# Optimization experiments

Hardware: AMD Instinct MI355X
Metric: run time of the kernel (lower is better)

## Reference

```python
import jax, jax.numpy as jnp
import numpy as np

T, H, E, F, K, FS = 2048, 2048, 64, 512, 8, 512


def setup_inputs() -> dict:
    key = jax.random.key(0)
    ks = jax.random.split(key, 6)
    s = 0.02
    return {
        "hidden_states": jax.random.normal(ks[0], (T, H), jnp.float32),
        # merged gate: E router logits + 1 shared-expert gate logit
        "W_gate": jax.random.normal(ks[1], (H, E + 1), jnp.float32) * s,
        # per-expert merged gate_up proj: [E, H, 2F]
        "W_gate_up": jax.random.normal(ks[2], (E, H, 2 * F), jnp.float32) * s,
        "W_down": jax.random.normal(ks[3], (E, F, H), jnp.float32) * s,
        # shared expert
        "Ws_gate_up": jax.random.normal(ks[4], (H, 2 * FS), jnp.float32) * s,
        "Ws_down": jax.random.normal(ks[5], (FS, H), jnp.float32) * s,
    }


def reference(hidden_states, W_gate, W_gate_up, W_down, Ws_gate_up, Ws_down):
    x = hidden_states  # [T, H]
    logits_all = x @ W_gate                      # [T, E+1]
    router_logits = logits_all[:, :E]
    shared_gate_logit = logits_all[:, E:]        # [T, 1]

    # FusedMoE routing: softmax -> top_k -> renormalize (norm_topk_prob=True)
    probs = jax.nn.softmax(router_logits.astype(jnp.float32), axis=-1)
    topk_w, topk_idx = jax.lax.top_k(probs, K)   # [T, K]
    topk_w = topk_w / jnp.sum(topk_w, axis=-1, keepdims=True)
    # dense combine weights [T, E] (zero for unselected experts)
    combine = jnp.zeros((T, E), probs.dtype).at[
        jnp.arange(T)[:, None], topk_idx].set(topk_w)

    # grouped expert GEMMs (dense reference: every expert sees all tokens,
    # combine-weights zero-out unrouted pairs)
    gu = jnp.einsum('th,ehf->etf', x, W_gate_up)   # [E, T, 2F]
    g, u = jnp.split(gu, 2, axis=-1)
    act = jax.nn.silu(g) * u                       # [E, T, F]
    # apply combine weight before down-proj to avoid [E, T, H] intermediate
    act = act * combine.T[:, :, None].astype(act.dtype)
    routed = jnp.einsum('etf,efh->th', act, W_down)  # [T, H]

    # shared expert (Qwen3NextMLP with sigmoid expert_gate)
    sgu = x @ Ws_gate_up                           # [T, 2FS]
    sg, su = jnp.split(sgu, 2, axis=-1)
    shared = (jax.nn.silu(sg) * su) @ Ws_down      # [T, H]
    shared = jax.nn.sigmoid(shared_gate_logit) * shared

    return shared + routed.astype(x.dtype)
```

## Files before the change

### kernel.cpp

```cpp
#include <hip/hip_runtime.h>
#include <hip/hip_bf16.h>
#include <math.h>

#define T_TOK 2048
#define H_DIM 2048
#define E_NUM 64
#define F_DIM 512
#define K_TOP 8
#define FS_DIM 512
#define NROWS (T_TOK * K_TOP)

typedef __attribute__((ext_vector_type(8))) short short8v;
typedef __attribute__((ext_vector_type(4))) float f32x4;

static __device__ __forceinline__ unsigned short f2bf(float f) {
    unsigned int u = __float_as_uint(f);
    u += 0x7fff + ((u >> 16) & 1);
    return (unsigned short)(u >> 16);
}

#define BCHUNK(row, k8) ((((k8) ^ ((row) + ((row) >> 3)))) & 7)
#define ASWZ(row) (((row) + ((row) >> 3)) & 7)

typedef const unsigned int __attribute__((address_space(1))) gu32;
typedef unsigned int __attribute__((address_space(3))) lu32;
#define GLDS16(gsrc, ldst) \
    __builtin_amdgcn_global_load_lds((gu32*)(gsrc), (lu32*)(ldst), 16, 0, 0)

__global__ __launch_bounds__(256) void cvt_bf16_kernel(
    const float* __restrict__ in, unsigned short* __restrict__ out, int n8)
{
    int i = blockIdx.x * 256 + threadIdx.x;
    if (i < n8) {
        const float4* p = (const float4*)(in + (size_t)i * 8);
        float4 v0 = p[0], v1 = p[1];
        ushort4 a = make_ushort4(f2bf(v0.x), f2bf(v0.y), f2bf(v0.z), f2bf(v0.w));
        ushort4 b = make_ushort4(f2bf(v1.x), f2bf(v1.y), f2bf(v1.z), f2bf(v1.w));
        ushort4* q = (ushort4*)(out + (size_t)i * 8);
        q[0] = a; q[1] = b;
    }
}

__global__ __launch_bounds__(64) void router_kernel(
    const float* __restrict__ x, const float* __restrict__ Wg,
    int* __restrict__ topk_idx, float* __restrict__ topk_w,
    float* __restrict__ sgate, int* __restrict__ counts)
{
    const int t = blockIdx.x;
    const int lane = threadIdx.x;
    const float* xr = x + (size_t)t * H_DIM;

    float a0 = 0.f, a1 = 0.f, a2 = 0.f, a3 = 0.f;
    for (int h = 0; h < H_DIM; h += 4) {
        float4 xv = *(const float4*)&xr[h];
        a0 += xv.x * Wg[(h + 0) * 65 + lane];
        a1 += xv.y * Wg[(h + 1) * 65 + lane];
        a2 += xv.z * Wg[(h + 2) * 65 + lane];
        a3 += xv.w * Wg[(h + 3) * 65 + lane];
    }
    float logit = (a0 + a1) + (a2 + a3);

    float a64 = 0.f;
    for (int h = lane; h < H_DIM; h += 64) a64 += xr[h] * Wg[h * 65 + 64];
#pragma unroll
    for (int off = 32; off >= 1; off >>= 1) a64 += __shfl_xor(a64, off);

    float v = logit;
    float selv[K_TOP]; int seli[K_TOP];
#pragma unroll
    for (int k = 0; k < K_TOP; ++k) {
        float mv = v; int mi = lane;
#pragma unroll
        for (int off = 32; off >= 1; off >>= 1) {
            float ov = __shfl_xor(mv, off);
            int   oi = __shfl_xor(mi, off);
            if (ov > mv || (ov == mv && oi < mi)) { mv = ov; mi = oi; }
        }
        selv[k] = mv; seli[k] = mi;
        if (lane == mi) v = -INFINITY;
    }

    if (lane == 0) {
        float m = selv[0];
        float w[K_TOP]; float s = 0.f;
#pragma unroll
        for (int k = 0; k < K_TOP; ++k) { w[k] = __expf(selv[k] - m); s += w[k]; }
        float inv = 1.f / s;
#pragma unroll
        for (int k = 0; k < K_TOP; ++k) {
            topk_idx[t * K_TOP + k] = seli[k];
            topk_w[t * K_TOP + k] = w[k] * inv;
            atomicAdd(&counts[seli[k]], 1);
        }
        sgate[t] = 1.f / (1.f + __expf(-a64));
    }
}

__global__ __launch_bounds__(256) void bucket_kernel(
    const int* __restrict__ topk_idx, const float* __restrict__ topk_w,
    const int* __restrict__ counts, int* __restrict__ offsets,
    int* __restrict__ bucket_tok, float* __restrict__ bucket_w)
{
    const int e = blockIdx.x, thr = threadIdx.x;
    __shared__ int cnt[256];
    __shared__ int base_s;
    const int q0 = thr * 64;
    int c = 0;
    for (int q = 0; q < 64; ++q) c += (topk_idx[q0 + q] == e) ? 1 : 0;
    cnt[thr] = c;
    __syncthreads();
    if (thr == 0) {
        int off = 0;
        for (int i = 0; i < e; ++i) off += counts[i];
        offsets[e] = off;
        base_s = off;
        int run = 0;
        for (int i = 0; i < 256; ++i) { int tval = cnt[i]; cnt[i] = run; run += tval; }
    }
    __syncthreads();
    int pos = base_s + cnt[thr];
    for (int q = 0; q < 64; ++q) {
        int pp = q0 + q;
        if (topk_idx[pp] == e) {
            bucket_tok[pos] = pp >> 3;
            bucket_w[pos] = topk_w[pp];
            ++pos;
        }
    }
}

template<bool ROUTED>
__global__ __launch_bounds__(256, 2) void gu_mfma_kernel(
    const unsigned short* __restrict__ xb,
    const float* __restrict__ Wall,
    const int* __restrict__ counts, const int* __restrict__ offsets,
    const int* __restrict__ bucket_tok, const float* __restrict__ bucket_w,
    unsigned short* __restrict__ actout)
{
    constexpr int BM = 128;
    __shared__ __align__(16) unsigned short As[2][BM * 64];
    __shared__ __align__(16) unsigned short Bs[2][128 * 64];
    __shared__ int   toksS[BM];
    __shared__ float twsS[BM];

    const int tid  = threadIdx.x;
    const int lane = tid & 63;
    const int wid  = tid >> 6;
    const int wm = wid >> 1, wn = wid & 1;
    const int lrow = lane & 15, lhi = lane >> 4;

    int cblk, ne, base;
    const float* W;
    if (ROUTED) {
        int nw = (blockIdx.x & 7) * ((int)gridDim.x >> 3) + (blockIdx.x >> 3);
        int e = nw >> 3; cblk = nw & 7;
        ne = counts[e]; base = offsets[e];
        W = Wall + (size_t)e * H_DIM * (2 * F_DIM);
    } else {
        cblk = blockIdx.x;
        ne = T_TOK; base = 0;
        W = Wall;
    }
    const int c0 = cblk * 64;

    const int n4 = (tid >> 3) * 4;
    const int kq = (tid & 7) * 8;
    const int grp = n4 >> 5;
    const int srccol = c0 + (grp >> 1) * 32 + (n4 & 31) + ((grp & 1) ? F_DIM : 0);
    int wrB[4];
#pragma unroll
    for (int cc = 0; cc < 4; ++cc) {
        int n = n4 + cc;
        wrB[cc] = n * 64 + BCHUNK(n, kq >> 3) * 8;
    }
    int rdB[4][2];
#pragma unroll
    for (int fn = 0; fn < 4; ++fn) {
        int r = wn * 64 + fn * 16 + lrow;
#pragma unroll
        for (int ks = 0; ks < 2; ++ks) {
            int kc = ks * 4 + lhi;
            rdB[fn][ks] = r * 64 + BCHUNK(r, kc) * 8;
        }
    }
    int rdA[4][2];
#pragma unroll
    for (int fm = 0; fm < 4; ++fm) {
        int arow = wm * 64 + fm * 16 + lrow;
#pragma unroll
        for (int ks = 0; ks < 2; ++ks) {
            int kc = ks * 4 + lhi;
            rdA[fm][ks] = arow * 64 + ((kc ^ ASWZ(arow)) & 7) * 8;
        }
    }
    const int NT = H_DIM / 64;

    const int m0_beg = ROUTED ? 0 : blockIdx.y * BM;
    const int m0_end = ROUTED ? ne : m0_beg + BM;

    for (int m0 = m0_beg; m0 < m0_end; m0 += BM) {
        __syncthreads();
        if (tid < BM) {
            int idx = m0 + tid; bool v = idx < ne;
            if (ROUTED) {
                toksS[tid] = v ? bucket_tok[base + idx] : bucket_tok[base];
                twsS[tid]  = v ? bucket_w[base + idx] : 0.f;
            } else {
                toksS[tid] = v ? idx : (T_TOK - 1);
                twsS[tid]  = 1.f;
            }
        }
        __syncthreads();

        int asrc[4];
#pragma unroll
        for (int i = 0; i < 4; ++i) {
            int row = wid * 32 + i * 8 + (lane >> 3);
            asrc[i] = toksS[row] * H_DIM + (((lane & 7) ^ ASWZ(row)) << 3);
        }

        f32x4 acc[4][4];
#pragma unroll
        for (int i = 0; i < 4; ++i)
#pragma unroll
            for (int j = 0; j < 4; ++j) acc[i][j] = (f32x4){0.f, 0.f, 0.f, 0.f};

        float4 bq[8];
#pragma unroll
        for (int j = 0; j < 8; ++j)
            bq[j] = *(const float4*)&W[(size_t)(kq + j) * (2 * F_DIM) + srccol];
#pragma unroll
        for (int cc = 0; cc < 4; ++cc) {
            short8v pk;
#pragma unroll
            for (int j = 0; j < 8; ++j)
                pk[j] = (short)f2bf(((const float*)&bq[j])[cc]);
            *(short8v*)&Bs[0][wrB[cc]] = pk;
        }
#pragma unroll
        for (int j = 0; j < 8; ++j)
            bq[j] = *(const float4*)&W[(size_t)(64 + kq + j) * (2 * F_DIM) + srccol];
#pragma unroll
        for (int i = 0; i < 4; ++i)
            GLDS16(xb + asrc[i], &As[0][(wid * 32 + i * 8) * 64]);
        __syncthreads();

        for (int kt = 0; kt < NT; ++kt) {
            const int k0 = kt * 64;
            if (kt + 1 < NT) {
#pragma unroll
                for (int i = 0; i < 4; ++i)
                    GLDS16(xb + asrc[i] + k0 + 64, &As[(kt + 1) & 1][(wid * 32 + i * 8) * 64]);
                unsigned short* nB = Bs[(kt + 1) & 1];
#pragma unroll
                for (int cc = 0; cc < 4; ++cc) {
                    short8v pk;
#pragma unroll
                    for (int j = 0; j < 8; ++j)
                        pk[j] = (short)f2bf(((const float*)&bq[j])[cc]);
                    *(short8v*)&nB[wrB[cc]] = pk;
                }
                int knx = (kt + 2 < NT) ? (k0 + 128) : (k0 + 64);
#pragma unroll
                for (int j = 0; j < 8; ++j)
                    bq[j] = *(const float4*)&W[(size_t)(knx + kq + j) * (2 * F_DIM) + srccol];
            }
            __builtin_amdgcn_sched_barrier(0);
            const unsigned short* A_ = As[kt & 1];
            const unsigned short* B_ = Bs[kt & 1];
            __builtin_amdgcn_s_setprio(1);
#pragma unroll
            for (int ks = 0; ks < 2; ++ks) {
                short8v bf[4];
#pragma unroll
                for (int fn = 0; fn < 4; ++fn) bf[fn] = *(const short8v*)&B_[rdB[fn][ks]];
#pragma unroll
                for (int fm = 0; fm < 4; ++fm) {
                    short8v af = *(const short8v*)&A_[rdA[fm][ks]];
#pragma unroll
                    for (int fn = 0; fn < 4; ++fn)
                        acc[fm][fn] = __builtin_amdgcn_mfma_f32_16x16x32_bf16(
                            af, bf[fn], acc[fm][fn], 0, 0, 0);
                }
            }
            __builtin_amdgcn_s_setprio(0);
            __syncthreads();
        }

#pragma unroll
        for (int fm = 0; fm < 4; ++fm) {
#pragma unroll
            for (int p = 0; p < 2; ++p) {
                const int acol = c0 + wn * 32 + p * 16 + lrow;
#pragma unroll
                for (int i = 0; i < 4; ++i) {
                    int ml = wm * 64 + fm * 16 + lhi * 4 + i;
                    int idx = m0 + ml;
                    if (idx < ne) {
                        float gv = acc[fm][p][i], uv = acc[fm][p + 2][i];
                        float sg = gv / (1.f + __expf(-gv));
                        float val = sg * uv * twsS[ml];
                        size_t orow = ROUTED ? (size_t)(base + idx) : (size_t)idx;
                        actout[orow * F_DIM + acol] = f2bf(val);
                    }
                }
            }
        }
    }
}

template<bool ROUTED>
__global__ __launch_bounds__(256, 2) void down_mfma_kernel(
    const unsigned short* __restrict__ actb,
    const float* __restrict__ Wall,
    const int* __restrict__ counts, const int* __restrict__ offsets,
    const int* __restrict__ bucket_tok, const float* __restrict__ sgate,
    float* __restrict__ out)
{
    constexpr int BM = 128;
    __shared__ __align__(16) unsigned short As[2][BM * 64];
    __shared__ __align__(16) unsigned short Bs[2][128 * 64];
    __shared__ int   toksS[BM];
    __shared__ float sgS[BM];

    const int tid  = threadIdx.x;
    const int lane = tid & 63;
    const int wid  = tid >> 6;
    const int wm = wid >> 1, wn = wid & 1;
    const int lrow = lane & 15, lhi = lane >> 4;

    int cblk, ne, base;
    const float* W;
    if (ROUTED) {
        int nw = (blockIdx.x & 7) * ((int)gridDim.x >> 3) + (blockIdx.x >> 3);
        int e = nw >> 4; cblk = nw & 15;
        ne = counts[e]; base = offsets[e];
        W = Wall + (size_t)e * F_DIM * H_DIM;
    } else {
        cblk = blockIdx.x;
        ne = T_TOK; base = 0;
        W = Wall;
    }
    const int c0 = cblk * 128;

    const int n4 = (tid >> 3) * 4;
    const int kq = (tid & 7) * 8;
    const int srccol = c0 + n4;
    int wrB[4];
#pragma unroll
    for (int cc = 0; cc < 4; ++cc) {
        int n = n4 + cc;
        wrB[cc] = n * 64 + BCHUNK(n, kq >> 3) * 8;
    }
    int rdB[4][2];
#pragma unroll
    for (int fn = 0; fn < 4; ++fn) {
        int r = wn * 64 + fn * 16 + lrow;
#pragma unroll
        for (int ks = 0; ks < 2; ++ks) {
            int kc = ks * 4 + lhi;
            rdB[fn][ks] = r * 64 + BCHUNK(r, kc) * 8;
        }
    }
    int rdA[4][2];
#pragma unroll
    for (int fm = 0; fm < 4; ++fm) {
        int arow = wm * 64 + fm * 16 + lrow;
#pragma unroll
        for (int ks = 0; ks < 2; ++ks) {
            int kc = ks * 4 + lhi;
            rdA[fm][ks] = arow * 64 + ((kc ^ ASWZ(arow)) & 7) * 8;
        }
    }
    const int NT = F_DIM / 64;

    const int m0_beg = ROUTED ? 0 : blockIdx.y * BM;
    const int m0_end = ROUTED ? ne : m0_beg + BM;

    for (int m0 = m0_beg; m0 < m0_end; m0 += BM) {
        __syncthreads();
        if (tid < BM) {
            int idx = m0 + tid;
            if (ROUTED) {
                toksS[tid] = (idx < ne) ? bucket_tok[base + idx] : 0;
            } else {
                sgS[tid] = sgate[(idx < ne) ? idx : (T_TOK - 1)];
            }
        }
        __syncthreads();

        int asrc[4];
#pragma unroll
        for (int i = 0; i < 4; ++i) {
            int row = wid * 32 + i * 8 + (lane >> 3);
            int grow = ROUTED ? min(base + m0 + row, NROWS - 1)
                              : min(m0 + row, T_TOK - 1);
            asrc[i] = grow * F_DIM + (((lane & 7) ^ ASWZ(row)) << 3);
        }

        f32x4 acc[4][4];
#pragma unroll
        for (int i = 0; i < 4; ++i)
#pragma unroll
            for (int j = 0; j < 4; ++j) acc[i][j] = (f32x4){0.f, 0.f, 0.f, 0.f};

        float4 bq[8];
#pragma unroll
        for (int j = 0; j < 8; ++j)
            bq[j] = *(const float4*)&W[(size_t)(kq + j) * H_DIM + srccol];
#pragma unroll
        for (int cc = 0; cc < 4; ++cc) {
            short8v pk;
#pragma unroll
            for (int j = 0; j < 8; ++j)
                pk[j] = (short)f2bf(((const float*)&bq[j])[cc]);
            *(short8v*)&Bs[0][wrB[cc]] = pk;
        }
#pragma unroll
        for (int j = 0; j < 8; ++j)
            bq[j] = *(const float4*)&W[(size_t)(64 + kq + j) * H_DIM + srccol];
#pragma unroll
        for (int i = 0; i < 4; ++i)
            GLDS16(actb + asrc[i], &As[0][(wid * 32 + i * 8) * 64]);
        __syncthreads();

        for (int kt = 0; kt < NT; ++kt) {
            const int k0 = kt * 64;
            if (kt + 1 < NT) {
#pragma unroll
                for (int i = 0; i < 4; ++i)
                    GLDS16(actb + asrc[i] + k0 + 64, &As[(kt + 1) & 1][(wid * 32 + i * 8) * 64]);
                unsigned short* nB = Bs[(kt + 1) & 1];
#pragma unroll
                for (int cc = 0; cc < 4; ++cc) {
                    short8v pk;
#pragma unroll
                    for (int j = 0; j < 8; ++j)
                        pk[j] = (short)f2bf(((const float*)&bq[j])[cc]);
                    *(short8v*)&nB[wrB[cc]] = pk;
                }
                int knx = (kt + 2 < NT) ? (k0 + 128) : (k0 + 64);
#pragma unroll
                for (int j = 0; j < 8; ++j)
                    bq[j] = *(const float4*)&W[(size_t)(knx + kq + j) * H_DIM + srccol];
            }
            __builtin_amdgcn_sched_barrier(0);
            const unsigned short* A_ = As[kt & 1];
            const unsigned short* B_ = Bs[kt & 1];
            __builtin_amdgcn_s_setprio(1);
#pragma unroll
            for (int ks = 0; ks < 2; ++ks) {
                short8v bf[4];
#pragma unroll
                for (int fn = 0; fn < 4; ++fn) bf[fn] = *(const short8v*)&B_[rdB[fn][ks]];
#pragma unroll
                for (int fm = 0; fm < 4; ++fm) {
                    short8v af = *(const short8v*)&A_[rdA[fm][ks]];
#pragma unroll
                    for (int fn = 0; fn < 4; ++fn)
                        acc[fm][fn] = __builtin_amdgcn_mfma_f32_16x16x32_bf16(
                            af, bf[fn], acc[fm][fn], 0, 0, 0);
                }
            }
            __builtin_amdgcn_s_setprio(0);
            __syncthreads();
        }

#pragma unroll
        for (int fm = 0; fm < 4; ++fm) {
#pragma unroll
            for (int fn = 0; fn < 4; ++fn) {
                int col = c0 + wn * 64 + fn * 16 + lrow;
#pragma unroll
                for (int i = 0; i < 4; ++i) {
                    int ml = wm * 64 + fm * 16 + lhi * 4 + i;
                    int idx = m0 + ml;
                    if (idx < ne) {
                        if (ROUTED)
                            atomicAdd(&out[(size_t)toksS[ml] * H_DIM + col], acc[fm][fn][i]);
                        else
                            out[(size_t)idx * H_DIM + col] = sgS[ml] * acc[fm][fn][i];
                    }
                }
            }
        }
    }
}

extern "C" void kernel_launch(void* const* d_in, const int* in_sizes, int n_in,
                              void* d_out, int out_size, void* d_ws, size_t ws_size,
                              hipStream_t stream) {
    const float* x    = (const float*)d_in[0];
    const float* Wg   = (const float*)d_in[1];
    const float* Wgu  = (const float*)d_in[2];
    const float* Wd   = (const float*)d_in[3];
    const float* Wsgu = (const float*)d_in[4];
    const float* Wsd  = (const float*)d_in[5];
    float* out = (float*)d_out;

    char* p = (char*)d_ws;
    auto alloc = [&](size_t bytes) {
        char* r = p;
        p += (bytes + 255) & ~(size_t)255;
        return r;
    };
    int*   topk_idx   = (int*)  alloc((size_t)T_TOK * K_TOP * sizeof(int));
    float* topk_w     = (float*)alloc((size_t)T_TOK * K_TOP * sizeof(float));
    float* sgate      = (float*)alloc((size_t)T_TOK * sizeof(float));
    int*   counts     = (int*)  alloc((size_t)E_NUM * sizeof(int));
    int*   offsets    = (int*)  alloc((size_t)E_NUM * sizeof(int));
    int*   bucket_tok = (int*)  alloc((size_t)NROWS * sizeof(int));
    float* bucket_w   = (float*)alloc((size_t)NROWS * sizeof(float));
    unsigned short* xb    = (unsigned short*)alloc((size_t)T_TOK * H_DIM * 2);
    unsigned short* act_r = (unsigned short*)alloc((size_t)NROWS * F_DIM * 2);
    unsigned short* act_s = (unsigned short*)alloc((size_t)T_TOK * FS_DIM * 2);

    hipMemsetAsync(counts, 0, E_NUM * sizeof(int), stream);
    cvt_bf16_kernel<<<(T_TOK * H_DIM / 8 + 255) / 256, 256, 0, stream>>>(x, xb, T_TOK * H_DIM / 8);
    router_kernel<<<T_TOK, 64, 0, stream>>>(x, Wg, topk_idx, topk_w, sgate, counts);
    bucket_kernel<<<E_NUM, 256, 0, stream>>>(topk_idx, topk_w, counts, offsets, bucket_tok, bucket_w);

    gu_mfma_kernel<true><<<8 * E_NUM, 256, 0, stream>>>(
        xb, Wgu, counts, offsets, bucket_tok, bucket_w, act_r);
    gu_mfma_kernel<false><<<dim3(8, T_TOK / 128), 256, 0, stream>>>(
        xb, Wsgu, counts, offsets, bucket_tok, bucket_w, act_s);

    down_mfma_kernel<false><<<dim3(16, T_TOK / 128), 256, 0, stream>>>(
        act_s, Wsd, counts, offsets, bucket_tok, sgate, out);
    down_mfma_kernel<true><<<16 * E_NUM, 256, 0, stream>>>(
        act_r, Wd, counts, offsets, bucket_tok, sgate, out);
}
```

Before: 746.1 us.

## Pre-transpose weights to bf16 and load B tiles via direct global-to-LDS

Adds a transpose-and-convert kernel that writes all expert and shared weights as bf16 in [N, K] layout before the GEMMs. The gate-up and down GEMM kernels then load B tiles with global_load_lds and a swizzle, like A, instead of loading fp32 through registers and converting in the inner loop. The pipeline becomes a two-stage prefetch governed by explicit vmcnt waits and raw barriers. The cost is an extra pass over about 800 MB of fp32 weights on every call, plus new workspace, in exchange for halving weight bytes in the GEMMs and freeing registers and VALU work.

```diff
diff --git a/kernel.cpp b/kernel.cpp
--- a/kernel.cpp
+++ b/kernel.cpp
@@ -19,13 +19,13 @@
     return (unsigned short)(u >> 16);
 }
 
-#define BCHUNK(row, k8) ((((k8) ^ ((row) + ((row) >> 3)))) & 7)
 #define ASWZ(row) (((row) + ((row) >> 3)) & 7)
 
 typedef const unsigned int __attribute__((address_space(1))) gu32;
 typedef unsigned int __attribute__((address_space(3))) lu32;
 #define GLDS16(gsrc, ldst) \
     __builtin_amdgcn_global_load_lds((gu32*)(gsrc), (lu32*)(ldst), 16, 0, 0)
+#define SB0() __builtin_amdgcn_sched_barrier(0)
 
 __global__ __launch_bounds__(256) void cvt_bf16_kernel(
     const float* __restrict__ in, unsigned short* __restrict__ out, int n8)
@@ -129,10 +129,38 @@
     }
 }
 
+__global__ __launch_bounds__(256) void transpose_cvt_kernel(
+    const float* __restrict__ in, unsigned short* __restrict__ out,
+    int R, int C)
+{
+    const int e = blockIdx.z;
+    in  += (size_t)e * R * C;
+    out += (size_t)e * R * C;
+    const int c0 = blockIdx.x * 64, r0 = blockIdx.y * 64;
+    __shared__ unsigned short tile[64][72];
+    const int t = threadIdx.x;
+    const int cc = (t & 15) * 4;
+#pragma unroll
+    for (int i = 0; i < 4; ++i) {
+        int r = (t >> 4) + i * 16;
+        float4 v = *(const float4*)&in[(size_t)(r0 + r) * C + c0 + cc];
+        tile[cc + 0][r] = f2bf(v.x);
+        tile[cc + 1][r] = f2bf(v.y);
+        tile[cc + 2][r] = f2bf(v.z);
+        tile[cc + 3][r] = f2bf(v.w);
+    }
+    __syncthreads();
+    const int c = t >> 2, j = t & 3;
+    uint4 v0 = *(const uint4*)&tile[c][j * 16];
+    uint4 v1 = *(const uint4*)&tile[c][j * 16 + 8];
+    uint4* dst = (uint4*)&out[(size_t)(c0 + c) * R + r0 + j * 16];
+    dst[0] = v0; dst[1] = v1;
+}
+
 template<bool ROUTED>
 __global__ __launch_bounds__(256, 2) void gu_mfma_kernel(
     const unsigned short* __restrict__ xb,
-    const float* __restrict__ Wall,
+    const unsigned short* __restrict__ WT,
     const int* __restrict__ counts, const int* __restrict__ offsets,
     const int* __restrict__ bucket_tok, const float* __restrict__ bucket_w,
     unsigned short* __restrict__ actout)
@@ -149,38 +177,26 @@
     const int wm = wid >> 1, wn = wid & 1;
     const int lrow = lane & 15, lhi = lane >> 4;
 
-    int cblk, ne, base;
-    const float* W;
+    int cblk, ne, base, e;
     if (ROUTED) {
         int nw = (blockIdx.x & 7) * ((int)gridDim.x >> 3) + (blockIdx.x >> 3);
-        int e = nw >> 3; cblk = nw & 7;
+        e = nw >> 3; cblk = nw & 7;
         ne = counts[e]; base = offsets[e];
-        W = Wall + (size_t)e * H_DIM * (2 * F_DIM);
     } else {
-        cblk = blockIdx.x;
+        e = E_NUM; cblk = blockIdx.x;
         ne = T_TOK; base = 0;
-        W = Wall;
     }
     const int c0 = cblk * 64;
-
-    const int n4 = (tid >> 3) * 4;
-    const int kq = (tid & 7) * 8;
-    const int grp = n4 >> 5;
-    const int srccol = c0 + (grp >> 1) * 32 + (n4 & 31) + ((grp & 1) ? F_DIM : 0);
-    int wrB[4];
-#pragma unroll
-    for (int cc = 0; cc < 4; ++cc) {
-        int n = n4 + cc;
-        wrB[cc] = n * 64 + BCHUNK(n, kq >> 3) * 8;
-    }
+    const unsigned short* We = WT + (size_t)e * (2 * F_DIM) * H_DIM;
+
     int rdB[4][2];
 #pragma unroll
     for (int fn = 0; fn < 4; ++fn) {
-        int r = wn * 64 + fn * 16 + lrow;
+        int r = ((fn & 1) ? 16 : 0) + wn * 32 + lrow + ((fn >> 1) ? 64 : 0);
 #pragma unroll
         for (int ks = 0; ks < 2; ++ks) {
             int kc = ks * 4 + lhi;
-            rdB[fn][ks] = r * 64 + BCHUNK(r, kc) * 8;
+            rdB[fn][ks] = r * 64 + ((kc ^ ASWZ(r)) & 7) * 8;
         }
     }
     int rdA[4][2];
@@ -192,6 +208,13 @@
             int kc = ks * 4 + lhi;
             rdA[fm][ks] = arow * 64 + ((kc ^ ASWZ(arow)) & 7) * 8;
         }
+    }
+    int bsrc[4];
+#pragma unroll
+    for (int i = 0; i < 4; ++i) {
+        int n = wid * 32 + i * 8 + (lane >> 3);
+        int grow = (n < 64) ? (c0 + n) : (F_DIM + c0 + (n - 64));
+        bsrc[i] = grow * H_DIM + (((lane & 7) ^ ASWZ(n)) << 3);
     }
     const int NT = H_DIM / 64;
 
@@ -225,47 +248,22 @@
 #pragma unroll
             for (int j = 0; j < 4; ++j) acc[i][j] = (f32x4){0.f, 0.f, 0.f, 0.f};
 
-        float4 bq[8];
-#pragma unroll
-        for (int j = 0; j < 8; ++j)
-            bq[j] = *(const float4*)&W[(size_t)(kq + j) * (2 * F_DIM) + srccol];
-#pragma unroll
-        for (int cc = 0; cc < 4; ++cc) {
-            short8v pk;
-#pragma unroll
-            for (int j = 0; j < 8; ++j)
-                pk[j] = (short)f2bf(((const float*)&bq[j])[cc]);
-            *(short8v*)&Bs[0][wrB[cc]] = pk;
-        }
-#pragma unroll
-        for (int j = 0; j < 8; ++j)
-            bq[j] = *(const float4*)&W[(size_t)(64 + kq + j) * (2 * F_DIM) + srccol];
-#pragma unroll
-        for (int i = 0; i < 4; ++i)
-            GLDS16(xb + asrc[i], &As[0][(wid * 32 + i * 8) * 64]);
-        __syncthreads();
+#pragma unroll
+        for (int i = 0; i < 4; ++i) GLDS16(xb + asrc[i], &As[0][(wid * 32 + i * 8) * 64]);
+#pragma unroll
+        for (int i = 0; i < 4; ++i) GLDS16(We + bsrc[i], &Bs[0][(wid * 32 + i * 8) * 64]);
+#pragma unroll
+        for (int i = 0; i < 4; ++i) GLDS16(xb + asrc[i] + 64, &As[1][(wid * 32 + i * 8) * 64]);
+#pragma unroll
+        for (int i = 0; i < 4; ++i) GLDS16(We + bsrc[i] + 64, &Bs[1][(wid * 32 + i * 8) * 64]);
+        SB0();
 
         for (int kt = 0; kt < NT; ++kt) {
-            const int k0 = kt * 64;
-            if (kt + 1 < NT) {
-#pragma unroll
-                for (int i = 0; i < 4; ++i)
-                    GLDS16(xb + asrc[i] + k0 + 64, &As[(kt + 1) & 1][(wid * 32 + i * 8) * 64]);
-                unsigned short* nB = Bs[(kt + 1) & 1];
-#pragma unroll
-                for (int cc = 0; cc < 4; ++cc) {
-                    short8v pk;
-#pragma unroll
-                    for (int j = 0; j < 8; ++j)
-                        pk[j] = (short)f2bf(((const float*)&bq[j])[cc]);
-                    *(short8v*)&nB[wrB[cc]] = pk;
-                }
-                int knx = (kt + 2 < NT) ? (k0 + 128) : (k0 + 64);
-#pragma unroll
-                for (int j = 0; j < 8; ++j)
-                    bq[j] = *(const float4*)&W[(size_t)(knx + kq + j) * (2 * F_DIM) + srccol];
-            }
-            __builtin_amdgcn_sched_barrier(0);
+            if (kt + 1 < NT) asm volatile("s_waitcnt vmcnt(8)" ::: "memory");
+            else             asm volatile("s_waitcnt vmcnt(0)" ::: "memory");
+            SB0();
+            __builtin_amdgcn_s_barrier();
+            SB0();
             const unsigned short* A_ = As[kt & 1];
             const unsigned short* B_ = Bs[kt & 1];
             __builtin_amdgcn_s_setprio(1);
@@ -284,7 +282,19 @@
                 }
             }
             __builtin_amdgcn_s_setprio(0);
-            __syncthreads();
+            SB0();
+            __builtin_amdgcn_s_barrier();
+            SB0();
+            if (kt + 2 < NT) {
+                const int kn = (kt + 2) * 64;
+#pragma unroll
+                for (int i = 0; i < 4; ++i)
+                    GLDS16(xb + asrc[i] + kn, &As[kt & 1][(wid * 32 + i * 8) * 64]);
+#pragma unroll
+                for (int i = 0; i < 4; ++i)
+                    GLDS16(We + bsrc[i] + kn, &Bs[kt & 1][(wid * 32 + i * 8) * 64]);
+                SB0();
+            }
         }
 
 #pragma unroll
@@ -312,7 +322,7 @@
 template<bool ROUTED>
 __global__ __launch_bounds__(256, 2) void down_mfma_kernel(
     const unsigned short* __restrict__ actb,
-    const float* __restrict__ Wall,
+    const unsigned short* __restrict__ WT,
     const int* __restrict__ counts, const int* __restrict__ offsets,
     const int* __restrict__ bucket_tok, const float* __restrict__ sgate,
     float* __restrict__ out)
@@ -329,29 +339,18 @@
     const int wm = wid >> 1, wn = wid & 1;
     const int lrow = lane & 15, lhi = lane >> 4;
 
-    int cblk, ne, base;
-    const float* W;
+    int cblk, ne, base, e;
     if (ROUTED) {
         int nw = (blockIdx.x & 7) * ((int)gridDim.x >> 3) + (blockIdx.x >> 3);
-        int e = nw >> 4; cblk = nw & 15;
+        e = nw >> 4; cblk = nw & 15;
         ne = counts[e]; base = offsets[e];
-        W = Wall + (size_t)e * F_DIM * H_DIM;
     } else {
-        cblk = blockIdx.x;
+        e = E_NUM; cblk = blockIdx.x;
         ne = T_TOK; base = 0;
-        W = Wall;
     }
     const int c0 = cblk * 128;
-
-    const int n4 = (tid >> 3) * 4;
-    const int kq = (tid & 7) * 8;
-    const int srccol = c0 + n4;
-    int wrB[4];
-#pragma unroll
-    for (int cc = 0; cc < 4; ++cc) {
-        int n = n4 + cc;
-        wrB[cc] = n * 64 + BCHUNK(n, kq >> 3) * 8;
-    }
+    const unsigned short* We = WT + (size_t)e * H_DIM * F_DIM;
+
     int rdB[4][2];
 #pragma unroll
     for (int fn = 0; fn < 4; ++fn) {
@@ -359,7 +358,7 @@
 #pragma unroll
         for (int ks = 0; ks < 2; ++ks) {
             int kc = ks * 4 + lhi;
-            rdB[fn][ks] = r * 64 + BCHUNK(r, kc) * 8;
+            rdB[fn][ks] = r * 64 + ((kc ^ ASWZ(r)) & 7) * 8;
         }
     }
     int rdA[4][2];
@@ -371,6 +370,12 @@
             int kc = ks * 4 + lhi;
             rdA[fm][ks] = arow * 64 + ((kc ^ ASWZ(arow)) & 7) * 8;
         }
+    }
+    int bsrc[4];
+#pragma unroll
+    for (int i = 0; i < 4; ++i) {
+        int n = wid * 32 + i * 8 + (lane >> 3);
+        bsrc[i] = (c0 + n) * F_DIM + (((lane & 7) ^ ASWZ(n)) << 3);
     }
     const int NT = F_DIM / 64;
 
@@ -404,47 +409,22 @@
 #pragma unroll
             for (int j = 0; j < 4; ++j) acc[i][j] = (f32x4){0.f, 0.f, 0.f, 0.f};
 
-        float4 bq[8];
-#pragma unroll
-        for (int j = 0; j < 8; ++j)
-            bq[j] = *(const float4*)&W[(size_t)(kq + j) * H_DIM + srccol];
-#pragma unroll
-        for (int cc = 0; cc < 4; ++cc) {
-            short8v pk;
-#pragma unroll
-            for (int j = 0; j < 8; ++j)
-                pk[j] = (short)f2bf(((const float*)&bq[j])[cc]);
-            *(short8v*)&Bs[0][wrB[cc]] = pk;
-        }
-#pragma unroll
-        for (int j = 0; j < 8; ++j)
-            bq[j] = *(const float4*)&W[(size_t)(64 + kq + j) * H_DIM + srccol];
-#pragma unroll
-        for (int i = 0; i < 4; ++i)
-            GLDS16(actb + asrc[i], &As[0][(wid * 32 + i * 8) * 64]);
-        __syncthreads();
+#pragma unroll
+        for (int i = 0; i < 4; ++i) GLDS16(actb + asrc[i], &As[0][(wid * 32 + i * 8) * 64]);
+#pragma unroll
+        for (int i = 0; i < 4; ++i) GLDS16(We + bsrc[i], &Bs[0][(wid * 32 + i * 8) * 64]);
+#pragma unroll
+        for (int i = 0; i < 4; ++i) GLDS16(actb + asrc[i] + 64, &As[1][(wid * 32 + i * 8) * 64]);
+#pragma unroll
+        for (int i = 0; i < 4; ++i) GLDS16(We + bsrc[i] + 64, &Bs[1][(wid * 32 + i * 8) * 64]);
+        SB0();
 
         for (int kt = 0; kt < NT; ++kt) {
-            const int k0 = kt * 64;
-            if (kt + 1 < NT) {
-#pragma unroll
-                for (int i = 0; i < 4; ++i)
-                    GLDS16(actb + asrc[i] + k0 + 64, &As[(kt + 1) & 1][(wid * 32 + i * 8) * 64]);
-                unsigned short* nB = Bs[(kt + 1) & 1];
-#pragma unroll
-                for (int cc = 0; cc < 4; ++cc) {
-                    short8v pk;
-#pragma unroll
-                    for (int j = 0; j < 8; ++j)
-                        pk[j] = (short)f2bf(((const float*)&bq[j])[cc]);
-                    *(short8v*)&nB[wrB[cc]] = pk;
-                }
-                int knx = (kt + 2 < NT) ? (k0 + 128) : (k0 + 64);
-#pragma unroll
-                for (int j = 0; j < 8; ++j)
-                    bq[j] = *(const float4*)&W[(size_t)(knx + kq + j) * H_DIM + srccol];
-            }
-            __builtin_amdgcn_sched_barrier(0);
+            if (kt + 1 < NT) asm volatile("s_waitcnt vmcnt(8)" ::: "memory");
+            else             asm volatile("s_waitcnt vmcnt(0)" ::: "memory");
+            SB0();
+            __builtin_amdgcn_s_barrier();
+            SB0();
             const unsigned short* A_ = As[kt & 1];
             const unsigned short* B_ = Bs[kt & 1];
             __builtin_amdgcn_s_setprio(1);
@@ -463,7 +443,19 @@
                 }
             }
             __builtin_amdgcn_s_setprio(0);
-            __syncthreads();
+            SB0();
+            __builtin_amdgcn_s_barrier();
+            SB0();
+            if (kt + 2 < NT) {
+                const int kn = (kt + 2) * 64;
+#pragma unroll
+                for (int i = 0; i < 4; ++i)
+                    GLDS16(actb + asrc[i] + kn, &As[kt & 1][(wid * 32 + i * 8) * 64]);
+#pragma unroll
+                for (int i = 0; i < 4; ++i)
+                    GLDS16(We + bsrc[i] + kn, &Bs[kt & 1][(wid * 32 + i * 8) * 64]);
+                SB0();
+            }
         }
 
 #pragma unroll
@@ -514,19 +506,30 @@
     unsigned short* xb    = (unsigned short*)alloc((size_t)T_TOK * H_DIM * 2);
     unsigned short* act_r = (unsigned short*)alloc((size_t)NROWS * F_DIM * 2);
     unsigned short* act_s = (unsigned short*)alloc((size_t)T_TOK * FS_DIM * 2);
+    unsigned short* WTgu = (unsigned short*)alloc((size_t)65 * (2 * F_DIM) * H_DIM * 2);
+    unsigned short* WTd  = (unsigned short*)alloc((size_t)65 * H_DIM * F_DIM * 2);
 
     hipMemsetAsync(counts, 0, E_NUM * sizeof(int), stream);
     cvt_bf16_kernel<<<(T_TOK * H_DIM / 8 + 255) / 256, 256, 0, stream>>>(x, xb, T_TOK * H_DIM / 8);
     router_kernel<<<T_TOK, 64, 0, stream>>>(x, Wg, topk_idx, topk_w, sgate, counts);
     bucket_kernel<<<E_NUM, 256, 0, stream>>>(topk_idx, topk_w, counts, offsets, bucket_tok, bucket_w);
 
+    transpose_cvt_kernel<<<dim3((2 * F_DIM) / 64, H_DIM / 64, E_NUM), 256, 0, stream>>>(
+        Wgu, WTgu, H_DIM, 2 * F_DIM);
+    transpose_cvt_kernel<<<dim3((2 * FS_DIM) / 64, H_DIM / 64, 1), 256, 0, stream>>>(
+        Wsgu, WTgu + (size_t)64 * (2 * F_DIM) * H_DIM, H_DIM, 2 * FS_DIM);
+    transpose_cvt_kernel<<<dim3(H_DIM / 64, F_DIM / 64, E_NUM), 256, 0, stream>>>(
+        Wd, WTd, F_DIM, H_DIM);
+    transpose_cvt_kernel<<<dim3(H_DIM / 64, FS_DIM / 64, 1), 256, 0, stream>>>(
+        Wsd, WTd + (size_t)64 * H_DIM * F_DIM, FS_DIM, H_DIM);
+
     gu_mfma_kernel<true><<<8 * E_NUM, 256, 0, stream>>>(
-        xb, Wgu, counts, offsets, bucket_tok, bucket_w, act_r);
+        xb, WTgu, counts, offsets, bucket_tok, bucket_w, act_r);
     gu_mfma_kernel<false><<<dim3(8, T_TOK / 128), 256, 0, stream>>>(
-        xb, Wsgu, counts, offsets, bucket_tok, bucket_w, act_s);
+        xb, WTgu, counts, offsets, bucket_tok, bucket_w, act_s);
 
     down_mfma_kernel<false><<<dim3(16, T_TOK / 128), 256, 0, stream>>>(
-        act_s, Wsd, counts, offsets, bucket_tok, sgate, out);
+        act_s, WTd, counts, offsets, bucket_tok, sgate, out);
     down_mfma_kernel<true><<<16 * E_NUM, 256, 0, stream>>>(
-        act_r, Wd, counts, offsets, bucket_tok, sgate, out);
-}
+        act_r, WTd, counts, offsets, bucket_tok, sgate, out);
+}
```

New measurement: 792.7 us. +6.2%, slower.
